# Kernel optimization log

Hardware: AMD Instinct MI355X
Metric: run time of the kernel (lower is better)

## Reference

```python
import jax, jax.numpy as jnp
import numpy as np

B, S, E, C = 128, 256, 768, 4


def setup_inputs() -> dict:
    key = jax.random.key(0)
    ks = jax.random.split(key, 8)
    questions = jax.random.normal(ks[0], (B, E), dtype=jnp.float32)
    segments = jax.random.normal(ks[1], (B, S, E), dtype=jnp.float32)
    W1 = jax.random.normal(ks[2], (2 * E, E), dtype=jnp.float32) * 0.02
    b1 = jnp.zeros((E,), dtype=jnp.float32)
    W2 = jax.random.normal(ks[3], (E, E // 2), dtype=jnp.float32) * 0.02
    b2 = jnp.zeros((E // 2,), dtype=jnp.float32)
    W3 = jax.random.normal(ks[4], (E // 2, C), dtype=jnp.float32) * 0.02
    b3 = jnp.zeros((C,), dtype=jnp.float32)
    num_segments = jax.random.randint(ks[5], (B,), 1, S + 1, dtype=jnp.int32)
    return {"questions": questions, "segments": segments, "W1": W1, "b1": b1,
            "W2": W2, "b2": b2, "W3": W3, "b3": b3, "num_segments": num_segments}


def reference(questions, segments, W1, b1, W2, b2, W3, b3, num_segments):
    # --- MLP instance scores (call()): concat question emb with every segment emb ---
    q = jnp.broadcast_to(questions[:, None, :], segments.shape)      # [B,S,E]
    x = jnp.concatenate([q, segments], axis=-1)                      # [B,S,2E]
    h = jax.nn.gelu(x @ W1 + b1, approximate=False)                  # keras gelu is exact
    h = jax.nn.gelu(h @ W2 + b2, approximate=False)
    preds = jax.nn.softmax(h @ W3 + b3, axis=-1)                     # [B,S,C]

    # --- per-bag noisy-OR style aggregation (aggregate_loss inner math, vectorized) ---
    # In the TF code, for class cid: s_j = sum(preds[j,:cid]) (exclusive cumsum over
    # classes), and product_of_sum_prob ACCUMULATES across the i loop, so
    # update_i = preds[i,cid] * cumprod_i( prod_{j!=k} s_j ) (leave-one-out products).
    mask = jnp.arange(S)[None, :] < num_segments[:, None]            # [B,S]
    mC = mask[..., None]                                             # [B,S,1]
    s = jnp.cumsum(preds, axis=-1) - preds                           # exclusive cumsum, [B,S,C]
    s_m = jnp.where(mC, s, 1.0)                                      # padded -> multiplicative identity
    # leave-one-out product over the segment axis via prefix/suffix cumprods
    cp_f = jnp.cumprod(s_m, axis=1)
    prefix = jnp.concatenate([jnp.ones_like(s_m[:, :1]), cp_f[:, :-1]], axis=1)
    cp_b = jnp.cumprod(s_m[:, ::-1], axis=1)[:, ::-1]
    suffix = jnp.concatenate([cp_b[:, 1:], jnp.ones_like(s_m[:, :1])], axis=1)
    L = prefix * suffix                                              # prod_{j!=k} s_j, [B,S,C]
    cpL = jnp.cumprod(L, axis=1)                                     # running product over i (padding is at the end)
    sum_term = jnp.sum(jnp.where(mC, preds * cpL, 0.0), axis=1)      # [B,C]
    prod_term = jnp.prod(jnp.where(mC, preds, 1.0), axis=1)          # prod_i preds[i,cid]
    agg = sum_term / jnp.float32(C) + prod_term                      # bag_pred_agg_scores, [B,C]
    return agg
```

## Files before the change

kernel.cpp:

```cpp
#include <hip/hip_runtime.h>
#include <hip/hip_bf16.h>


typedef __attribute__((ext_vector_type(8))) short short8;
typedef __attribute__((ext_vector_type(8))) unsigned short ushort8;
typedef __attribute__((ext_vector_type(4))) float f32x4;
typedef __attribute__((ext_vector_type(16))) float f32x16;

__device__ __forceinline__ unsigned short f2bf(float f) {
    union { float f; unsigned int u; } c; c.f = f;
    unsigned int u = c.u;
    unsigned int r = (u + 0x7FFFu + ((u >> 16) & 1u)) >> 16;
    return (unsigned short)r;
}
__device__ __forceinline__ float bf2f(unsigned short u) {
    union { unsigned int u; float f; } c; c.u = ((unsigned int)u) << 16;
    return c.f;
}
__device__ __forceinline__ float gelu_fast(float x) {
    float x2 = x * x;
    float y2 = 1.5957691216057308f * (x + 0.044715f * x2 * x);
    float e = __expf(y2);
    float t = 1.0f - 2.0f * __builtin_amdgcn_rcpf(e + 1.0f);
    return 0.5f * x * (1.0f + t);
}

typedef const __attribute__((address_space(1))) void* gas_t;
typedef __attribute__((address_space(3))) void* las_t;
__device__ __forceinline__ void g2l16(const void* g, void* l) {
    __builtin_amdgcn_global_load_lds((gas_t)g, (las_t)l, 16, 0, 0);
}

#define PREP_Q    96
#define PREP_TR1E 240
#define PREP_TR2E 312
#define PREP_END  12600

__global__ __launch_bounds__(256) void prep_kernel(
    const float* __restrict__ segments, unsigned short* __restrict__ segB,
    const float* __restrict__ W1, unsigned short* __restrict__ W1t,
    const float* __restrict__ W2, unsigned short* __restrict__ W2t,
    const float* __restrict__ questions, float* __restrict__ qW1p)
{
    __shared__ __align__(16) char sh[16640];
    const int bid = blockIdx.x, tid = threadIdx.x;

    if (bid < PREP_Q) {
        const int s = bid / 24, rem = bid % 24;
        const int n0 = (rem % 12) * 64, m0 = (rem / 12) * 64;
        float (*As)[64] = (float(*)[64])sh;
        float (*Bs)[64] = (float(*)[64])(sh + 4096);
        const int tn = tid & 15, tm = tid >> 4;
        float acc[4][4] = {};
        const int la_m = tid >> 2;
        const int la_k = (tid & 3) << 2;
        const int lb_k = tid >> 4;
        const int lb_n = (tid & 15) << 2;
        const float* Aptr = questions + (size_t)(m0 + la_m) * 768 + la_k;
        const float* Bptr = W1 + (size_t)lb_k * 768 + n0 + lb_n;
        const int kbeg = s * 192, kend = kbeg + 192;
        for (int k0 = kbeg; k0 < kend; k0 += 16) {
            float4 av = *(const float4*)(Aptr + k0);
            float4 bv = *(const float4*)(Bptr + (size_t)k0 * 768);
            As[la_k + 0][la_m] = av.x;
            As[la_k + 1][la_m] = av.y;
            As[la_k + 2][la_m] = av.z;
            As[la_k + 3][la_m] = av.w;
            *(float4*)&Bs[lb_k][lb_n] = bv;
            __syncthreads();
            #pragma unroll
            for (int k = 0; k < 16; k++) {
                float4 a = *(const float4*)&As[k][tm << 2];
                float4 b = *(const float4*)&Bs[k][tn << 2];
                float ar[4] = {a.x, a.y, a.z, a.w};
                float br[4] = {b.x, b.y, b.z, b.w};
                #pragma unroll
                for (int i = 0; i < 4; i++)
                    #pragma unroll
                    for (int j = 0; j < 4; j++)
                        acc[i][j] += ar[i] * br[j];
            }
            __syncthreads();
        }
        float* outp = qW1p + (size_t)s * 128 * 768;
        #pragma unroll
        for (int i = 0; i < 4; i++) {
            int row = m0 + (tm << 2) + i;
            int colBase = n0 + (tn << 2);
            *(float4*)&outp[(size_t)row * 768 + colBase] =
                make_float4(acc[i][0], acc[i][1], acc[i][2], acc[i][3]);
        }
        return;
    }

    if (bid < PREP_TR2E) {
        const float* in; unsigned short* outp; int R, C, bx, by;
        if (bid < PREP_TR1E) {
            int idx = bid - PREP_Q; bx = idx % 12; by = idx / 12;
            in = W1 + 768 * 768; outp = W1t; R = 768; C = 768;
        } else {
            int idx = bid - PREP_TR1E; bx = idx % 6; by = idx / 6;
            in = W2; outp = W2t; R = 768; C = 384;
        }
        float (*t)[65] = (float(*)[65])sh;
        int r0 = by * 64, c0 = bx * 64;
        int tx = tid & 63, ty = tid >> 6;
        #pragma unroll
        for (int p = 0; p < 16; p++) {
            int row = ty * 16 + p;
            t[row][tx] = in[(size_t)(r0 + row) * C + c0 + tx];
        }
        __syncthreads();
        #pragma unroll
        for (int p = 0; p < 16; p++) {
            int orow = ty * 16 + p;
            outp[(size_t)(c0 + orow) * R + r0 + tx] = f2bf(t[tx][orow]);
        }
        return;
    }

    {
        long i = (long)(bid - PREP_TR2E) * 256 + tid;
        const float4* in = (const float4*)segments;
        float4 a = in[2 * i], b = in[2 * i + 1];
        ushort8 o;
        o[0] = f2bf(a.x); o[1] = f2bf(a.y); o[2] = f2bf(a.z); o[3] = f2bf(a.w);
        o[4] = f2bf(b.x); o[5] = f2bf(b.y); o[6] = f2bf(b.z); o[7] = f2bf(b.w);
        *(ushort8*)(segB + i * 8) = o;
    }
}

__global__ __launch_bounds__(256) void mfma_gemm_bt(
    const unsigned short* __restrict__ A,
    const unsigned short* __restrict__ Bt,
    const float* __restrict__ bias,
    const float* __restrict__ rowAdd,
    unsigned short* __restrict__ Cout,
    int M, int N, int K, int applyGelu)
{
    __shared__ __align__(16) unsigned short smem[128 * 128];
    unsigned short* As = smem;
    unsigned short* Bs = smem + 8192;
    const int tid = threadIdx.x;
    const int wave = tid >> 6, lane = tid & 63;
    const int m0 = blockIdx.y * 128, n0 = blockIdx.x * 128;
    const int wm = (wave & 1) * 64, wn = (wave >> 1) * 64;

    f32x16 acc[2][2] = {};

    const int srow = tid >> 3;
    const int schunk = (tid & 7) ^ (srow & 7);
    const unsigned short* Ag = A + (size_t)(m0 + srow) * K + schunk * 8;
    const unsigned short* Bg = Bt + (size_t)(n0 + srow) * K + schunk * 8;
    unsigned short* Al = As + tid * 8;
    unsigned short* Bl = Bs + tid * 8;

    const int fm = lane & 31, fq = lane >> 5;
    const int fs = fm & 7;

    for (int k0 = 0; k0 < K; k0 += 64) {
        #pragma unroll
        for (int r = 0; r < 4; r++) {
            g2l16(Ag + k0 + (size_t)(32 * r) * K, Al + r * 2048);
            g2l16(Bg + k0 + (size_t)(32 * r) * K, Bl + r * 2048);
        }
        __syncthreads();

        short8 af[2][4], bfr[2][4];
        #pragma unroll
        for (int i = 0; i < 2; i++)
            #pragma unroll
            for (int kh = 0; kh < 4; kh++)
                af[i][kh] = *(const short8*)
                    &As[(wm + i * 32 + fm) * 64 + (((kh << 1) | fq) ^ fs) * 8];
        #pragma unroll
        for (int j = 0; j < 2; j++)
            #pragma unroll
            for (int kh = 0; kh < 4; kh++)
                bfr[j][kh] = *(const short8*)
                    &Bs[(wn + j * 32 + fm) * 64 + (((kh << 1) | fq) ^ fs) * 8];
        #pragma unroll
        for (int kh = 0; kh < 4; kh++)
            #pragma unroll
            for (int i = 0; i < 2; i++)
                #pragma unroll
                for (int j = 0; j < 2; j++)
                    acc[i][j] = __builtin_amdgcn_mfma_f32_32x32x16_bf16(
                        af[i][kh], bfr[j][kh], acc[i][j], 0, 0, 0);
        __syncthreads();
    }

    const float* radd = rowAdd ? (rowAdd + (size_t)(m0 >> 8) * N) : nullptr;
    #pragma unroll
    for (int j = 0; j < 2; j++) {
        int coll = wn + j * 32 + fm;
        int col = n0 + coll;
        float add = bias ? bias[col] : 0.0f;
        if (radd)
            add += radd[col] + radd[col + 98304] +
                   radd[col + 2 * 98304] + radd[col + 3 * 98304];
        #pragma unroll
        for (int i = 0; i < 2; i++) {
            int rbase = wm + i * 32 + 4 * fq;
            #pragma unroll
            for (int reg = 0; reg < 16; reg++) {
                int rowl = rbase + (reg & 3) + 8 * (reg >> 2);
                float v = acc[i][j][reg] + add;
                if (applyGelu) v = gelu_fast(v);
                smem[rowl * 128 + coll] = f2bf(v);
            }
        }
    }
    __syncthreads();
    #pragma unroll
    for (int it = 0; it < 8; it++) {
        int idx = it * 256 + tid;
        int r = idx >> 4, cc = (idx & 15) * 8;
        *(ushort8*)&Cout[(size_t)(m0 + r) * N + n0 + cc] =
            *(const ushort8*)&smem[r * 128 + cc];
    }
}

__device__ __forceinline__ float4 f4mul(float4 a, float4 b) {
    return make_float4(a.x * b.x, a.y * b.y, a.z * b.z, a.w * b.w);
}
__device__ float4 scan_prod(float4 v, float4* buf, int tid) {
    __syncthreads();
    buf[tid] = v;
    __syncthreads();
    #pragma unroll
    for (int off = 1; off < 256; off <<= 1) {
        float4 o = (tid >= off) ? buf[tid - off] : make_float4(1.f, 1.f, 1.f, 1.f);
        __syncthreads();
        v = f4mul(v, o);
        buf[tid] = v;
        __syncthreads();
    }
    return v;
}

__global__ __launch_bounds__(256) void head_kernel(
    const unsigned short* __restrict__ H2, const float* __restrict__ W3,
    const float* __restrict__ b3, const int* __restrict__ nseg,
    float* __restrict__ out)
{
    __shared__ float4 buf[256];
    __shared__ float4 w3s[384];
    const int b = blockIdx.x, tid = threadIdx.x;
    for (int i = tid; i < 384; i += 256) w3s[i] = ((const float4*)W3)[i];
    __syncthreads();

    const unsigned short* hrow = H2 + (size_t)(b * 256 + tid) * 384;
    float4 acc = make_float4(b3[0], b3[1], b3[2], b3[3]);
    #pragma unroll
    for (int kk = 0; kk < 48; kk++) {
        ushort8 u = *(const ushort8*)(hrow + kk * 8);
        #pragma unroll
        for (int j = 0; j < 8; j++) {
            float h = bf2f(u[j]);
            float4 w = w3s[kk * 8 + j];
            acc.x += h * w.x; acc.y += h * w.y; acc.z += h * w.z; acc.w += h * w.w;
        }
    }
    float m = fmaxf(fmaxf(acc.x, acc.y), fmaxf(acc.z, acc.w));
    float e0 = __expf(acc.x - m), e1 = __expf(acc.y - m),
          e2 = __expf(acc.z - m), e3 = __expf(acc.w - m);
    float inv = 1.0f / (e0 + e1 + e2 + e3);
    float4 p = make_float4(e0 * inv, e1 * inv, e2 * inv, e3 * inv);

    const int n = nseg[b];
    const float4 ones = make_float4(1.f, 1.f, 1.f, 1.f);
    bool msk = tid < n;
    float s1 = p.x, s2 = s1 + p.y, s3 = s2 + p.z;
    float4 sm = msk ? make_float4(0.f, s1, s2, s3) : ones;

    scan_prod(sm, buf, tid);
    float4 pfx = (tid > 0) ? buf[tid - 1] : ones;
    __syncthreads();

    buf[255 - tid] = sm;
    __syncthreads();
    float4 rsm = buf[tid];
    scan_prod(rsm, buf, tid);
    float4 sfx = (tid < 255) ? buf[254 - tid] : ones;

    float4 L = f4mul(pfx, sfx);
    float4 cpL = scan_prod(L, buf, tid);

    float4 term = msk ? f4mul(p, cpL) : make_float4(0.f, 0.f, 0.f, 0.f);
    float4 pm = msk ? p : ones;

    __syncthreads();
    buf[tid] = term;
    __syncthreads();
    for (int off = 128; off > 0; off >>= 1) {
        if (tid < off) {
            float4 a = buf[tid], c = buf[tid + off];
            buf[tid] = make_float4(a.x + c.x, a.y + c.y, a.z + c.z, a.w + c.w);
        }
        __syncthreads();
    }
    float4 sum_t = buf[0];
    __syncthreads();

    buf[tid] = pm;
    __syncthreads();
    for (int off = 128; off > 0; off >>= 1) {
        if (tid < off) buf[tid] = f4mul(buf[tid], buf[tid + off]);
        __syncthreads();
    }
    if (tid == 0) {
        float4 pr = buf[0];
        ((float4*)out)[b] = make_float4(0.25f * sum_t.x + pr.x,
                                        0.25f * sum_t.y + pr.y,
                                        0.25f * sum_t.z + pr.z,
                                        0.25f * sum_t.w + pr.w);
    }
}

extern "C" void kernel_launch(void* const* d_in, const int* in_sizes, int n_in,
                              void* d_out, int out_size, void* d_ws, size_t ws_size,
                              hipStream_t stream) {
    (void)in_sizes; (void)n_in; (void)out_size; (void)ws_size;
    const float* questions = (const float*)d_in[0];
    const float* segments  = (const float*)d_in[1];
    const float* W1 = (const float*)d_in[2];
    const float* b1 = (const float*)d_in[3];
    const float* W2 = (const float*)d_in[4];
    const float* b2 = (const float*)d_in[5];
    const float* W3 = (const float*)d_in[6];
    const float* b3 = (const float*)d_in[7];
    const int*  nseg = (const int*)d_in[8];
    float* out = (float*)d_out;

    char* w = (char*)d_ws;
    float* qW1p = (float*)w;           w += (size_t)4 * 128 * 768 * 4;
    unsigned short* W1t = (unsigned short*)w; w += (size_t)768 * 768 * 2;
    unsigned short* W2t = (unsigned short*)w; w += (size_t)384 * 768 * 2;
    unsigned short* segB = (unsigned short*)w; w += (size_t)32768 * 768 * 2;
    unsigned short* H1b  = (unsigned short*)w; w += (size_t)32768 * 768 * 2;
    unsigned short* H2b  = (unsigned short*)w; w += (size_t)32768 * 384 * 2;

    prep_kernel<<<PREP_END, 256, 0, stream>>>(
        segments, segB, W1, W1t, W2, W2t, questions, qW1p);
    mfma_gemm_bt<<<dim3(6, 256), 256, 0, stream>>>(
        segB, W1t, b1, qW1p, H1b, 32768, 768, 768, 1);
    mfma_gemm_bt<<<dim3(3, 256), 256, 0, stream>>>(
        H1b, W2t, b2, nullptr, H2b, 32768, 384, 768, 1);
    head_kernel<<<128, 256, 0, stream>>>(H2b, W3, b3, nseg, out);
}
```

Measured before the change: 283.6 us.

## Load GEMM B fragments directly from global into registers, skip LDS staging

The weight (B) operand of the MFMA GEMM is now read by each wave straight from global memory into its register fragments instead of being staged through shared memory. Only the A tile goes through LDS. The grid is also transposed so that consecutive blocks walk along M while sharing the same weight column tile, which aims to improve L2 reuse of the weights. This removes half the LDS traffic and the LDS reads for B. In exchange, B loads become uncoalesced 16-byte per-lane reads, and each weight element is fetched twice, once by each of the two waves sharing a column band.

```diff
diff --git a/kernel.cpp b/kernel.cpp
--- a/kernel.cpp
+++ b/kernel.cpp
@@ -140,60 +140,58 @@
 {
     __shared__ __align__(16) unsigned short smem[128 * 128];
     unsigned short* As = smem;
-    unsigned short* Bs = smem + 8192;
     const int tid = threadIdx.x;
     const int wave = tid >> 6, lane = tid & 63;
-    const int m0 = blockIdx.y * 128, n0 = blockIdx.x * 128;
-    const int wm = (wave & 1) * 64, wn = (wave >> 1) * 64;
+    const int m0 = blockIdx.x * 128, n0 = blockIdx.y * 128;
+    const int wm = (wave & 1) * 64;
+    const int wcol = (wave >> 1) * 64;
 
     f32x16 acc[2][2] = {};
 
     const int srow = tid >> 3;
     const int schunk = (tid & 7) ^ (srow & 7);
     const unsigned short* Ag = A + (size_t)(m0 + srow) * K + schunk * 8;
-    const unsigned short* Bg = Bt + (size_t)(n0 + srow) * K + schunk * 8;
     unsigned short* Al = As + tid * 8;
-    unsigned short* Bl = Bs + tid * 8;
 
     const int fm = lane & 31, fq = lane >> 5;
     const int fs = fm & 7;
 
+    const unsigned short* Bgf = Bt + (size_t)(n0 + wcol + fm) * K + fq * 8;
+
     for (int k0 = 0; k0 < K; k0 += 64) {
-        #pragma unroll
-        for (int r = 0; r < 4; r++) {
+        short8 bfr[2][4];
+        #pragma unroll
+        for (int j = 0; j < 2; j++)
+            #pragma unroll
+            for (int kh = 0; kh < 4; kh++)
+                bfr[j][kh] = *(const short8*)(Bgf + (size_t)j * 32 * K + k0 + kh * 16);
+
+        #pragma unroll
+        for (int r = 0; r < 4; r++)
             g2l16(Ag + k0 + (size_t)(32 * r) * K, Al + r * 2048);
-            g2l16(Bg + k0 + (size_t)(32 * r) * K, Bl + r * 2048);
-        }
-        __syncthreads();
-
-        short8 af[2][4], bfr[2][4];
-        #pragma unroll
-        for (int i = 0; i < 2; i++)
-            #pragma unroll
-            for (int kh = 0; kh < 4; kh++)
-                af[i][kh] = *(const short8*)
-                    &As[(wm + i * 32 + fm) * 64 + (((kh << 1) | fq) ^ fs) * 8];
-        #pragma unroll
-        for (int j = 0; j < 2; j++)
-            #pragma unroll
-            for (int kh = 0; kh < 4; kh++)
-                bfr[j][kh] = *(const short8*)
-                    &Bs[(wn + j * 32 + fm) * 64 + (((kh << 1) | fq) ^ fs) * 8];
-        #pragma unroll
-        for (int kh = 0; kh < 4; kh++)
+        __syncthreads();
+
+        #pragma unroll
+        for (int kh = 0; kh < 4; kh++) {
+            const int kc = (((kh << 1) | fq) ^ fs) * 8;
+            short8 af[2];
+            #pragma unroll
+            for (int i = 0; i < 2; i++)
+                af[i] = *(const short8*)&As[(wm + i * 32 + fm) * 64 + kc];
             #pragma unroll
             for (int i = 0; i < 2; i++)
                 #pragma unroll
                 for (int j = 0; j < 2; j++)
                     acc[i][j] = __builtin_amdgcn_mfma_f32_32x32x16_bf16(
-                        af[i][kh], bfr[j][kh], acc[i][j], 0, 0, 0);
+                        af[i], bfr[j][kh], acc[i][j], 0, 0, 0);
+        }
         __syncthreads();
     }
 
     const float* radd = rowAdd ? (rowAdd + (size_t)(m0 >> 8) * N) : nullptr;
     #pragma unroll
     for (int j = 0; j < 2; j++) {
-        int coll = wn + j * 32 + fm;
+        int coll = wcol + j * 32 + fm;
         int col = n0 + coll;
         float add = bias ? bias[col] : 0.0f;
         if (radd)
@@ -343,9 +341,9 @@
 
     prep_kernel<<<PREP_END, 256, 0, stream>>>(
         segments, segB, W1, W1t, W2, W2t, questions, qW1p);
-    mfma_gemm_bt<<<dim3(6, 256), 256, 0, stream>>>(
+    mfma_gemm_bt<<<dim3(256, 6), 256, 0, stream>>>(
         segB, W1t, b1, qW1p, H1b, 32768, 768, 768, 1);
-    mfma_gemm_bt<<<dim3(3, 256), 256, 0, stream>>>(
+    mfma_gemm_bt<<<dim3(256, 3), 256, 0, stream>>>(
         H1b, W2t, b2, nullptr, H2b, 32768, 384, 768, 1);
     head_kernel<<<128, 256, 0, stream>>>(H2b, W3, b3, nseg, out);
 }
```

Result: slower. 323.3 us (+14.0%).

## Run the first-layer segment GEMM in FP8 with scaled MFMA

Applied to the files above, without the earlier changes.

Segments and the segment half of W1 are now converted to FP8 (E4M3) in the prep kernel instead of bf16. A new GEMM kernel feeds them to the gfx950 scaled 32x32x64 f8f6f4 MFMA with unit scales. The goal is to halve the bytes written and read for the largest operand and to raise matrix throughput. The cost is lower precision: segment values near 1 and weights around 0.02 lose mantissa bits, and the tiny weights may fall into FP8's subnormal range, which could hurt accuracy.

```diff
diff --git a/kernel.cpp b/kernel.cpp
--- a/kernel.cpp
+++ b/kernel.cpp
@@ -4,8 +4,9 @@
 
 typedef __attribute__((ext_vector_type(8))) short short8;
 typedef __attribute__((ext_vector_type(8))) unsigned short ushort8;
-typedef __attribute__((ext_vector_type(4))) float f32x4;
 typedef __attribute__((ext_vector_type(16))) float f32x16;
+typedef __attribute__((ext_vector_type(8))) int i32x8;
+typedef __attribute__((ext_vector_type(4))) int i32x4;
 
 __device__ __forceinline__ unsigned short f2bf(float f) {
     union { float f; unsigned int u; } c; c.f = f;
@@ -31,14 +32,19 @@
     __builtin_amdgcn_global_load_lds((gas_t)g, (las_t)l, 16, 0, 0);
 }
 
+__device__ __forceinline__ unsigned int f4_to_fp8x4(float a, float b, float c, float d) {
+    int lo = __builtin_amdgcn_cvt_pk_fp8_f32(a, b, 0, 0);
+    return (unsigned int)__builtin_amdgcn_cvt_pk_fp8_f32(c, d, lo, 1);
+}
+
 #define PREP_Q    96
 #define PREP_TR1E 240
 #define PREP_TR2E 312
 #define PREP_END  12600
 
 __global__ __launch_bounds__(256) void prep_kernel(
-    const float* __restrict__ segments, unsigned short* __restrict__ segB,
-    const float* __restrict__ W1, unsigned short* __restrict__ W1t,
+    const float* __restrict__ segments, unsigned char* __restrict__ segF8,
+    const float* __restrict__ W1, unsigned char* __restrict__ W1t8,
     const float* __restrict__ W2, unsigned short* __restrict__ W2t,
     const float* __restrict__ questions, float* __restrict__ qW1p)
 {
@@ -94,13 +100,13 @@
     }
 
     if (bid < PREP_TR2E) {
-        const float* in; unsigned short* outp; int R, C, bx, by;
+        const float* in; int R, C, bx, by, isF8;
         if (bid < PREP_TR1E) {
             int idx = bid - PREP_Q; bx = idx % 12; by = idx / 12;
-            in = W1 + 768 * 768; outp = W1t; R = 768; C = 768;
+            in = W1 + 768 * 768; R = 768; C = 768; isF8 = 1;
         } else {
             int idx = bid - PREP_TR1E; bx = idx % 6; by = idx / 6;
-            in = W2; outp = W2t; R = 768; C = 384;
+            in = W2; R = 768; C = 384; isF8 = 0;
         }
         float (*t)[65] = (float(*)[65])sh;
         int r0 = by * 64, c0 = bx * 64;
@@ -114,7 +120,13 @@
         #pragma unroll
         for (int p = 0; p < 16; p++) {
             int orow = ty * 16 + p;
-            outp[(size_t)(c0 + orow) * R + r0 + tx] = f2bf(t[tx][orow]);
+            float v = t[tx][orow];
+            if (isF8) {
+                W1t8[(size_t)(c0 + orow) * R + r0 + tx] =
+                    (unsigned char)(f4_to_fp8x4(v, 0.f, 0.f, 0.f) & 0xFF);
+            } else {
+                W2t[(size_t)(c0 + orow) * R + r0 + tx] = f2bf(v);
+            }
         }
         return;
     }
@@ -123,10 +135,98 @@
         long i = (long)(bid - PREP_TR2E) * 256 + tid;
         const float4* in = (const float4*)segments;
         float4 a = in[2 * i], b = in[2 * i + 1];
-        ushort8 o;
-        o[0] = f2bf(a.x); o[1] = f2bf(a.y); o[2] = f2bf(a.z); o[3] = f2bf(a.w);
-        o[4] = f2bf(b.x); o[5] = f2bf(b.y); o[6] = f2bf(b.z); o[7] = f2bf(b.w);
-        *(ushort8*)(segB + i * 8) = o;
+        unsigned int lo = f4_to_fp8x4(a.x, a.y, a.z, a.w);
+        unsigned int hi = f4_to_fp8x4(b.x, b.y, b.z, b.w);
+        *(uint2*)(segF8 + i * 8) = make_uint2(lo, hi);
+    }
+}
+
+__global__ __launch_bounds__(256) void mfma_gemm_f8(
+    const unsigned char* __restrict__ A8,
+    const unsigned char* __restrict__ Bt8,
+    const float* __restrict__ bias,
+    const float* __restrict__ rowAdd,
+    unsigned short* __restrict__ Cout,
+    int M, int N, int K)
+{
+    __shared__ __align__(16) unsigned char smem8[32768];
+    unsigned char* As = smem8;
+    unsigned char* Bs = smem8 + 8192;
+    const int tid = threadIdx.x;
+    const int wave = tid >> 6, lane = tid & 63;
+    const int m0 = blockIdx.y * 128, n0 = blockIdx.x * 128;
+    const int wm = (wave & 1) * 64, wn = (wave >> 1) * 64;
+
+    f32x16 acc[2][2] = {};
+
+    const int srow = tid >> 2;
+    const int schunk = (tid & 3) ^ ((srow >> 1) & 3);
+    const unsigned char* Ag = A8 + (size_t)(m0 + srow) * K + schunk * 16;
+    const unsigned char* Bg = Bt8 + (size_t)(n0 + srow) * K + schunk * 16;
+    unsigned char* Al = As + tid * 16;
+    unsigned char* Bl = Bs + tid * 16;
+
+    const int fm = lane & 31, fq = lane >> 5;
+
+    for (int k0 = 0; k0 < K; k0 += 64) {
+        g2l16(Ag + k0, Al);
+        g2l16(Ag + (size_t)64 * K + k0, Al + 4096);
+        g2l16(Bg + k0, Bl);
+        g2l16(Bg + (size_t)64 * K + k0, Bl + 4096);
+        __syncthreads();
+
+        i32x8 av[2], bv[2];
+        #pragma unroll
+        for (int i = 0; i < 2; i++) {
+            int rw = wm + i * 32 + fm, key = (rw >> 1) & 3;
+            i32x4 lo = *(const i32x4*)&As[rw * 64 + (((fq << 1) | 0) ^ key) * 16];
+            i32x4 hi = *(const i32x4*)&As[rw * 64 + (((fq << 1) | 1) ^ key) * 16];
+            av[i][0] = lo[0]; av[i][1] = lo[1]; av[i][2] = lo[2]; av[i][3] = lo[3];
+            av[i][4] = hi[0]; av[i][5] = hi[1]; av[i][6] = hi[2]; av[i][7] = hi[3];
+        }
+        #pragma unroll
+        for (int j = 0; j < 2; j++) {
+            int rw = wn + j * 32 + fm, key = (rw >> 1) & 3;
+            i32x4 lo = *(const i32x4*)&Bs[rw * 64 + (((fq << 1) | 0) ^ key) * 16];
+            i32x4 hi = *(const i32x4*)&Bs[rw * 64 + (((fq << 1) | 1) ^ key) * 16];
+            bv[j][0] = lo[0]; bv[j][1] = lo[1]; bv[j][2] = lo[2]; bv[j][3] = lo[3];
+            bv[j][4] = hi[0]; bv[j][5] = hi[1]; bv[j][6] = hi[2]; bv[j][7] = hi[3];
+        }
+        #pragma unroll
+        for (int i = 0; i < 2; i++)
+            #pragma unroll
+            for (int j = 0; j < 2; j++)
+                acc[i][j] = __builtin_amdgcn_mfma_scale_f32_32x32x64_f8f6f4(
+                    av[i], bv[j], acc[i][j], 0, 0,
+                    0, 127, 0, 127);
+        __syncthreads();
+    }
+
+    unsigned short* cst = (unsigned short*)smem8;
+    const float* radd = rowAdd + (size_t)(m0 >> 8) * N;
+    #pragma unroll
+    for (int j = 0; j < 2; j++) {
+        int coll = wn + j * 32 + fm;
+        int col = n0 + coll;
+        float add = bias[col] + radd[col] + radd[col + 98304] +
+                    radd[col + 2 * 98304] + radd[col + 3 * 98304];
+        #pragma unroll
+        for (int i = 0; i < 2; i++) {
+            int rbase = wm + i * 32 + 4 * fq;
+            #pragma unroll
+            for (int reg = 0; reg < 16; reg++) {
+                int rowl = rbase + (reg & 3) + 8 * (reg >> 2);
+                cst[rowl * 128 + coll] = f2bf(gelu_fast(acc[i][j][reg] + add));
+            }
+        }
+    }
+    __syncthreads();
+    #pragma unroll
+    for (int it = 0; it < 8; it++) {
+        int idx = it * 256 + tid;
+        int r = idx >> 4, cc = (idx & 15) * 8;
+        *(ushort8*)&Cout[(size_t)(m0 + r) * N + n0 + cc] =
+            *(const ushort8*)&cst[r * 128 + cc];
     }
 }
 
@@ -134,7 +234,6 @@
     const unsigned short* __restrict__ A,
     const unsigned short* __restrict__ Bt,
     const float* __restrict__ bias,
-    const float* __restrict__ rowAdd,
     unsigned short* __restrict__ Cout,
     int M, int N, int K, int applyGelu)
 {
@@ -190,15 +289,11 @@
         __syncthreads();
     }
 
-    const float* radd = rowAdd ? (rowAdd + (size_t)(m0 >> 8) * N) : nullptr;
     #pragma unroll
     for (int j = 0; j < 2; j++) {
         int coll = wn + j * 32 + fm;
         int col = n0 + coll;
         float add = bias ? bias[col] : 0.0f;
-        if (radd)
-            add += radd[col] + radd[col + 98304] +
-                   radd[col + 2 * 98304] + radd[col + 3 * 98304];
         #pragma unroll
         for (int i = 0; i < 2; i++) {
             int rbase = wm + i * 32 + 4 * fq;
@@ -334,18 +429,18 @@
     float* out = (float*)d_out;
 
     char* w = (char*)d_ws;
-    float* qW1p = (float*)w;           w += (size_t)4 * 128 * 768 * 4;
-    unsigned short* W1t = (unsigned short*)w; w += (size_t)768 * 768 * 2;
-    unsigned short* W2t = (unsigned short*)w; w += (size_t)384 * 768 * 2;
-    unsigned short* segB = (unsigned short*)w; w += (size_t)32768 * 768 * 2;
+    float* qW1p = (float*)w;                   w += (size_t)4 * 128 * 768 * 4;
+    unsigned char*  W1t8 = (unsigned char*)w;  w += (size_t)768 * 768;
+    unsigned short* W2t = (unsigned short*)w;  w += (size_t)384 * 768 * 2;
+    unsigned char*  segF8 = (unsigned char*)w; w += (size_t)32768 * 768;
     unsigned short* H1b  = (unsigned short*)w; w += (size_t)32768 * 768 * 2;
     unsigned short* H2b  = (unsigned short*)w; w += (size_t)32768 * 384 * 2;
 
     prep_kernel<<<PREP_END, 256, 0, stream>>>(
-        segments, segB, W1, W1t, W2, W2t, questions, qW1p);
-    mfma_gemm_bt<<<dim3(6, 256), 256, 0, stream>>>(
-        segB, W1t, b1, qW1p, H1b, 32768, 768, 768, 1);
+        segments, segF8, W1, W1t8, W2, W2t, questions, qW1p);
+    mfma_gemm_f8<<<dim3(6, 256), 256, 0, stream>>>(
+        segF8, W1t8, b1, qW1p, H1b, 32768, 768, 768);
     mfma_gemm_bt<<<dim3(3, 256), 256, 0, stream>>>(
-        H1b, W2t, b2, nullptr, H2b, 32768, 384, 768, 1);
+        H1b, W2t, b2, H2b, 32768, 384, 768, 1);
     head_kernel<<<128, 256, 0, stream>>>(H2b, W3, b3, nseg, out);
 }
```

Result: faster. 254.6 us (-10.3%).
